# Performance work log

Hardware: AMD Instinct MI355X
Metric: run time of the kernel (lower is better)

## Reference

```python
import jax, jax.numpy as jnp
import numpy as np

B, L, HC, D = 4, 4096, 4, 1024
K, DIL = 4, 2
EPS = 1e-5
C = HC * D
PAD = (K - 1) * DIL


def setup_inputs() -> dict:
    key = jax.random.key(0)
    k1, k2, k3 = jax.random.split(key, 3)
    x = jax.random.normal(k1, (B, L, HC, D), dtype=jnp.float32)
    # RMSNorm affine weights, one per chunk (torch init: ones; randomize slightly for a
    # non-trivial baseline)
    norm_weight = 1.0 + 0.02 * jax.random.normal(k2, (HC, D), dtype=jnp.float32)
    # depthwise conv weight [C, 1, K] (torch init is zeros; use small random values so
    # the kernel-correctness baseline is non-degenerate)
    conv_weight = 0.1 * jax.random.normal(k3, (C, 1, K), dtype=jnp.float32)
    return {"x": x, "norm_weight": norm_weight, "conv_weight": conv_weight}


def reference(x, norm_weight, conv_weight):
    # per-chunk RMSNorm over last dim: [B, L, HC, D]
    ms = jnp.mean(jnp.square(x), axis=-1, keepdims=True)
    xn = x * jax.lax.rsqrt(ms + EPS) * norm_weight[None, None, :, :]
    # concat chunks along feature dim -> [B, L, C], then to [B, C, L]
    xc = xn.reshape(B, L, C).transpose(0, 2, 1)
    # depthwise dilated causal conv1d: left-pad (K-1)*DIL, output length L
    y = jax.lax.conv_general_dilated(
        xc, conv_weight,
        window_strides=(1,),
        padding=((PAD, 0),),
        rhs_dilation=(DIL,),
        feature_group_count=C,
        dimension_numbers=("NCH", "OIH", "NCH"),
    )
    y = jax.nn.silu(y)
    # back to [B, L, HC, D]
    return y.transpose(0, 2, 1).reshape(B, L, HC, D)
```

## Files before the change

kernel.cpp:

```cpp
#include <hip/hip_runtime.h>

namespace {

constexpr int NB = 4, L = 4096, HC = 4, D = 1024, KW = 4;
constexpr int PAD = 6;
constexpr float EPS = 1e-5f;
constexpr int ST = 2;
constexpr int NSTEP = 32;
constexpr int CL = ST * NSTEP;
constexpr int NT = L / CL;
constexpr int BDIM = 256;

typedef float f32x4 __attribute__((ext_vector_type(4)));

#define LGKM_BARRIER() do {                                    \
    asm volatile("s_waitcnt lgkmcnt(0)" ::: "memory");         \
    __builtin_amdgcn_s_barrier();                              \
} while (0)

__device__ __forceinline__ void stage16(const float* g, float* l) {
    __builtin_amdgcn_global_load_lds(
        (const __attribute__((address_space(1))) void*)g,
        (__attribute__((address_space(3))) void*)l, 16, 0, 0);
}

__global__ __launch_bounds__(BDIM, 4) void engram_shortconv_v9(
    const float* __restrict__ x,
    const float* __restrict__ nw,
    const float* __restrict__ cw,
    float* __restrict__ out)
{
    __shared__ float s_buf[3][ST][D];
    __shared__ float s_part[PAD][BDIM];
    __shared__ float s_inv2[2][ST];
    __shared__ float s_invh[PAD];

    const int lblk = (blockIdx.x & 7) * 128 + (blockIdx.x >> 3);
    const int t    = lblk % NT;
    const int hc   = (lblk / NT) % HC;
    const int b    = lblk / (NT * HC);
    const int l0   = t * CL;

    const int tid  = threadIdx.x;
    const int wave = tid >> 6;
    const int lane = tid & 63;

    const size_t rs = (size_t)HC * D;
    const float* xcol = x   + ((size_t)b * L * HC + (size_t)hc) * D + tid * 4;
    float*       ocol = out + ((size_t)b * L * HC + (size_t)hc) * D + tid * 4;

    const float4 nw4 = *(const float4*)(nw + (size_t)hc * D + tid * 4);
    float4 cwv[4];
    #pragma unroll
    for (int j = 0; j < 4; ++j)
        cwv[j] = *(const float4*)(cw + ((size_t)hc * D + tid * 4 + j) * KW);

    float win[PAD][4];
    #pragma unroll
    for (int r = 0; r < PAD; ++r) {
        const int l = l0 - PAD + r;
        float4 v = make_float4(0.f, 0.f, 0.f, 0.f);
        if (l >= 0) v = *(const float4*)(xcol + (size_t)l * rs);
        win[r][0] = v.x; win[r][1] = v.y; win[r][2] = v.z; win[r][3] = v.w;
    }

    #pragma unroll
    for (int s = 0; s < 3; ++s)
        #pragma unroll
        for (int r = 0; r < ST; ++r)
            stage16(xcol + (size_t)(l0 + s * ST + r) * rs, &s_buf[s][r][wave * 256]);

    float wk[4][4];
    {
        const float gv[4] = { nw4.x, nw4.y, nw4.z, nw4.w };
        #pragma unroll
        for (int j = 0; j < 4; ++j) {
            wk[j][0] = cwv[j].x * gv[j]; wk[j][1] = cwv[j].y * gv[j];
            wk[j][2] = cwv[j].z * gv[j]; wk[j][3] = cwv[j].w * gv[j];
        }
    }

    #pragma unroll
    for (int r = 0; r < PAD; ++r)
        s_part[r][tid] = win[r][0]*win[r][0] + win[r][1]*win[r][1]
                       + win[r][2]*win[r][2] + win[r][3]*win[r][3];
    LGKM_BARRIER();
    {
        int rr = wave;
        float s1 = s_part[rr][lane]       + s_part[rr][lane + 64]
                 + s_part[rr][lane + 128] + s_part[rr][lane + 192];
        #pragma unroll
        for (int off = 32; off >= 1; off >>= 1) s1 += __shfl_xor(s1, off);
        if (lane == 0) s_invh[rr] = rsqrtf(s1 * (1.0f / D) + EPS);
        rr = wave + 4;
        if (rr < PAD) {
            float s2 = s_part[rr][lane]       + s_part[rr][lane + 64]
                     + s_part[rr][lane + 128] + s_part[rr][lane + 192];
            #pragma unroll
            for (int off = 32; off >= 1; off >>= 1) s2 += __shfl_xor(s2, off);
            if (lane == 0) s_invh[rr] = rsqrtf(s2 * (1.0f / D) + EPS);
        }
    }
    LGKM_BARRIER();
    #pragma unroll
    for (int r = 0; r < PAD; ++r) {
        const float iv = s_invh[r];
        win[r][0] *= iv; win[r][1] *= iv; win[r][2] *= iv; win[r][3] *= iv;
    }

    asm volatile("s_waitcnt vmcnt(2)" ::: "memory");
    __builtin_amdgcn_s_barrier();
    {
        const int row = wave & 1;
        const float* rp = &s_buf[0][row][0];
        float ss = 0.0f;
        #pragma unroll
        for (int q = 0; q < 4; ++q) {
            const f32x4 v = *(const f32x4*)(rp + lane * 4 + q * 256);
            ss = fmaf(v.x, v.x, fmaf(v.y, v.y, fmaf(v.z, v.z, fmaf(v.w, v.w, ss))));
        }
        #pragma unroll
        for (int off = 32; off >= 1; off >>= 1) ss += __shfl_xor(ss, off);
        if (lane == 0) s_inv2[0][row] = rsqrtf(ss * (1.0f / D) + EPS);
    }
    LGKM_BARRIER();

    float* p0 = &s_buf[0][0][0];
    float* p1 = &s_buf[1][0][0];
    float* p2 = &s_buf[2][0][0];

    #pragma unroll 1
    for (int s = 0; s < NSTEP; ++s) {
        if (s < NSTEP - 1) {
            const int row = wave & 1;
            const float* rp = p1 + row * D;
            float ss = 0.0f;
            #pragma unroll
            for (int q = 0; q < 4; ++q) {
                const f32x4 v = *(const f32x4*)(rp + lane * 4 + q * 256);
                ss = fmaf(v.x, v.x, fmaf(v.y, v.y, fmaf(v.z, v.z, fmaf(v.w, v.w, ss))));
            }
            #pragma unroll
            for (int off = 32; off >= 1; off >>= 1) ss += __shfl_xor(ss, off);
            if (lane == 0) s_inv2[(s + 1) & 1][row] = rsqrtf(ss * (1.0f / D) + EPS);
        }

        const int base = l0 + s * ST;
        float cur[ST][4];
        #pragma unroll
        for (int r = 0; r < ST; ++r) {
            const f32x4 v = *(const f32x4*)(p0 + r * D + tid * 4);
            const float iv = s_inv2[s & 1][r];
            cur[r][0] = v.x * iv; cur[r][1] = v.y * iv;
            cur[r][2] = v.z * iv; cur[r][3] = v.w * iv;
        }
        float ov[ST][4];
        #pragma unroll
        for (int i = 0; i < ST; ++i) {
            #pragma unroll
            for (int j = 0; j < 4; ++j) {
                float a = 0.0f;
                #pragma unroll
                for (int k = 0; k < 4; ++k) {
                    const int rel = i - 6 + 2 * k;
                    const float xv = (rel < 0) ? win[6 + rel][j] : cur[rel][j];
                    a = fmaf(wk[j][k], xv, a);
                }
                ov[i][j] = a / (1.0f + __expf(-a));
            }
        }

        #pragma unroll
        for (int r = 0; r < PAD - ST; ++r) {
            win[r][0] = win[r + ST][0]; win[r][1] = win[r + ST][1];
            win[r][2] = win[r + ST][2]; win[r][3] = win[r + ST][3];
        }
        #pragma unroll
        for (int r = 0; r < ST; ++r) {
            win[PAD - ST + r][0] = cur[r][0]; win[PAD - ST + r][1] = cur[r][1];
            win[PAD - ST + r][2] = cur[r][2]; win[PAD - ST + r][3] = cur[r][3];
        }

        if (s < NSTEP - 3) {
            asm volatile("s_waitcnt lgkmcnt(0)" ::: "memory");
            __builtin_amdgcn_sched_barrier(0);
            #pragma unroll
            for (int r = 0; r < ST; ++r)
                stage16(xcol + (size_t)(l0 + (s + 3) * ST + r) * rs,
                        p0 + r * D + wave * 256);
            __builtin_amdgcn_sched_barrier(0);
        }

        #pragma unroll
        for (int i = 0; i < ST; ++i) {
            f32x4 o = { ov[i][0], ov[i][1], ov[i][2], ov[i][3] };
            __builtin_nontemporal_store(o, (f32x4*)(ocol + (size_t)(base + i) * rs));
        }

        if (s < NSTEP - 1) {
            if (s <= NSTEP - 4)      asm volatile("s_waitcnt vmcnt(6)" ::: "memory");
            else if (s == NSTEP - 3) asm volatile("s_waitcnt vmcnt(4)" ::: "memory");
            LGKM_BARRIER();
        }

        float* tmp = p0; p0 = p1; p1 = p2; p2 = tmp;
    }
}

}

extern "C" void kernel_launch(void* const* d_in, const int* in_sizes, int n_in,
                              void* d_out, int out_size, void* d_ws, size_t ws_size,
                              hipStream_t stream) {
    const float* x  = (const float*)d_in[0];
    const float* nw = (const float*)d_in[1];
    const float* cw = (const float*)d_in[2];
    float* out = (float*)d_out;

    const int nblocks = NB * HC * NT;
    engram_shortconv_v9<<<dim3(nblocks), dim3(BDIM), 0, stream>>>(x, nw, cw, out);
}
```

Measured before the change: 96.85 us.

## Halve per-block chunk length, shrink halo reduction scratch, raise occupancy

Halves the number of time steps per block, which doubles the block count and shortens each block's serial chain. The launch-bound occupancy hint goes from 4 to 6, and the block-index swizzle now uses a computed constant. The halo RMS reduction becomes a per-wave shuffle reduction followed by a small cross-wave sum, which shrinks the s_part LDS array from 6x256 to 6x4 and frees LDS for more resident blocks. In exchange, each block re-reads a 6-row halo that is a larger fraction of its work, and the register cap may cause spills.

```diff
diff --git a/kernel.cpp b/kernel.cpp
--- a/kernel.cpp
+++ b/kernel.cpp
@@ -6,10 +6,12 @@
 constexpr int PAD = 6;
 constexpr float EPS = 1e-5f;
 constexpr int ST = 2;
-constexpr int NSTEP = 32;
+constexpr int NSTEP = 16;
 constexpr int CL = ST * NSTEP;
 constexpr int NT = L / CL;
 constexpr int BDIM = 256;
+constexpr int NBLK = NB * HC * NT;
+constexpr int CPX = NBLK / 8;
 
 typedef float f32x4 __attribute__((ext_vector_type(4)));
 
@@ -24,18 +26,18 @@
         (__attribute__((address_space(3))) void*)l, 16, 0, 0);
 }
 
-__global__ __launch_bounds__(BDIM, 4) void engram_shortconv_v9(
+__global__ __launch_bounds__(BDIM, 6) void engram_shortconv_v10(
     const float* __restrict__ x,
     const float* __restrict__ nw,
     const float* __restrict__ cw,
     float* __restrict__ out)
 {
     __shared__ float s_buf[3][ST][D];
-    __shared__ float s_part[PAD][BDIM];
+    __shared__ float s_part[PAD][4];
     __shared__ float s_inv2[2][ST];
     __shared__ float s_invh[PAD];
 
-    const int lblk = (blockIdx.x & 7) * 128 + (blockIdx.x >> 3);
+    const int lblk = (blockIdx.x & 7) * CPX + (blockIdx.x >> 3);
     const int t    = lblk % NT;
     const int hc   = (lblk / NT) % HC;
     const int b    = lblk / (NT * HC);
@@ -81,25 +83,18 @@
     }
 
     #pragma unroll
-    for (int r = 0; r < PAD; ++r)
-        s_part[r][tid] = win[r][0]*win[r][0] + win[r][1]*win[r][1]
-                       + win[r][2]*win[r][2] + win[r][3]*win[r][3];
+    for (int r = 0; r < PAD; ++r) {
+        float ss = fmaf(win[r][0], win[r][0], fmaf(win[r][1], win[r][1],
+                   fmaf(win[r][2], win[r][2], win[r][3] * win[r][3])));
+        #pragma unroll
+        for (int off = 32; off >= 1; off >>= 1) ss += __shfl_xor(ss, off);
+        if (lane == 0) s_part[r][wave] = ss;
+    }
     LGKM_BARRIER();
-    {
-        int rr = wave;
-        float s1 = s_part[rr][lane]       + s_part[rr][lane + 64]
-                 + s_part[rr][lane + 128] + s_part[rr][lane + 192];
-        #pragma unroll
-        for (int off = 32; off >= 1; off >>= 1) s1 += __shfl_xor(s1, off);
-        if (lane == 0) s_invh[rr] = rsqrtf(s1 * (1.0f / D) + EPS);
-        rr = wave + 4;
-        if (rr < PAD) {
-            float s2 = s_part[rr][lane]       + s_part[rr][lane + 64]
-                     + s_part[rr][lane + 128] + s_part[rr][lane + 192];
-            #pragma unroll
-            for (int off = 32; off >= 1; off >>= 1) s2 += __shfl_xor(s2, off);
-            if (lane == 0) s_invh[rr] = rsqrtf(s2 * (1.0f / D) + EPS);
-        }
+    if (wave == 0 && lane < PAD) {
+        const float s = s_part[lane][0] + s_part[lane][1]
+                      + s_part[lane][2] + s_part[lane][3];
+        s_invh[lane] = rsqrtf(s * (1.0f / D) + EPS);
     }
     LGKM_BARRIER();
     #pragma unroll
@@ -217,6 +212,5 @@
     const float* cw = (const float*)d_in[2];
     float* out = (float*)d_out;
 
-    const int nblocks = NB * HC * NT;
-    engram_shortconv_v9<<<dim3(nblocks), dim3(BDIM), 0, stream>>>(x, nw, cw, out);
-}
+    engram_shortconv_v10<<<dim3(NBLK), dim3(BDIM), 0, stream>>>(x, nw, cw, out);
+}
```

After: 101.6 us. 4.9% more time.
